# Kernel tuning notes

Hardware: AMD Instinct MI355X
Metric: run time of the kernel (lower is better)

The kernel has to match this reference:

```python
import jax, jax.numpy as jnp
import numpy as np
import itertools


def _rot24():
    # all 3x3 signed permutation matrices with det +1 -> 24 cube rotations
    mats = []
    I = np.eye(3)
    for perm in itertools.permutations(range(3)):
        P = I[list(perm)]
        for signs in itertools.product([1.0, -1.0], repeat=3):
            M = P * np.array(signs)[:, None]
            if np.linalg.det(M) > 0:
                mats.append(M)
    return np.stack(mats)  # (24, 3, 3)


def compute_spatial_pair_orbits():
    # O acts on the 24 positions (regular rep). Orbit of pair (i,j) under the
    # diagonal action g:(i,j)->(gi,gj) is indexed by the group element i^-1 j.
    R = _rot24()
    n = R.shape[0]
    orb = np.zeros((n, n), dtype=np.int64)
    for i in range(n):
        for j in range(n):
            M = R[i].T @ R[j]
            orb[i, j] = int(np.argmin(np.abs(R - M).sum(axis=(1, 2))))
    return orb, n  # (24, 24), 24 orbits


def compute_color_pair_orbits():
    # S6 on color pairs: orbit 0 = same color (a==b), orbit 1 = different
    a = np.arange(6)
    orb = (a[:, None] != a[None, :]).astype(np.int64)
    return orb, 2  # (6, 6), 2 orbits


K_IN = 64
K_OUT = 64
BATCH = 64


def setup_inputs() -> dict:
    key = jax.random.key(0)
    k_x, k_w = jax.random.split(key)
    sp_orbit_np, n_sp = compute_spatial_pair_orbits()
    co_orbit_np, n_co = compute_color_pair_orbits()
    x = jax.random.normal(k_x, (BATCH, 24, K_IN * 6), dtype=jnp.float32)
    # kaiming_uniform with a=sqrt(5): bound = sqrt(6 / ((1 + a^2) * fan_in)),
    # fan_in = k_in * n_sp * n_co (dims after the first of weight)
    fan_in = K_IN * n_sp * n_co
    bound = float(np.sqrt(6.0 / ((1.0 + 5.0) * fan_in)))
    weight = jax.random.uniform(k_w, (K_OUT, K_IN, n_sp, n_co),
                                dtype=jnp.float32, minval=-bound, maxval=bound)
    bias = jnp.zeros((K_OUT,), dtype=jnp.float32)
    return {
        "x": x,
        "weight": weight,
        "bias": bias,
        "sp_orbit": jnp.asarray(sp_orbit_np),
        "co_orbit": jnp.asarray(co_orbit_np),
    }


def reference(x, weight, bias, sp_orbit, co_orbit):
    B = x.shape[0]
    k_out, k_in = weight.shape[0], weight.shape[1]
    xr = x.reshape(B, 24, k_in, 6)                 # (B, j, ki, c)
    kernel = weight[:, :, sp_orbit, :]             # (ko, ki, 24, 24, n_co)
    kernel_full = kernel[:, :, :, :, co_orbit]     # (ko, ki, 24, 24, 6, 6)
    out = jnp.einsum('bjkc,okijdc->biod', xr, kernel_full)
    out = out + bias[None, None, :, None]
    return out.reshape(B, 24, k_out * 6)
```

## Files before the change

kernel.cpp:

```cpp
#include <hip/hip_runtime.h>


typedef short bf16x8 __attribute__((ext_vector_type(8)));
typedef float f32x4 __attribute__((ext_vector_type(4)));

static __device__ inline short f2bf(float f) {
    unsigned u = __builtin_bit_cast(unsigned, f);
    unsigned r = (u + 0x7fffu + ((u >> 16) & 1u)) >> 16;
    return (short)r;
}

#define MFMA16(a, b, c) __builtin_amdgcn_mfma_f32_16x16x32_bf16(a, b, c, 0, 0, 0)

__global__ __launch_bounds__(512) void prep_kernel(const float* __restrict__ weight,
                                                   const float* __restrict__ x,
                                                   short* __restrict__ Wfrag,
                                                   short* __restrict__ Bfrag) {
    __shared__ float xs[9216];
    __shared__ float Ss[1536];
    const int t = threadIdx.x;
    const int blk = blockIdx.x;

    if (blk < 24) {
        const int s = blk;
        const int o = t >> 3;
        const int k0 = (t & 7) << 3;
        bf16x8 vd, v1;
        #pragma unroll
        for (int e = 0; e < 8; ++e) {
            const float2 wv = *(const float2*)(weight + ((size_t)((o * 64 + k0 + e) * 24 + s) << 1));
            vd[e] = f2bf(wv.x - wv.y);
            v1[e] = f2bf(wv.y);
        }
        const int lane_f = (o & 15) | (((k0 >> 3) & 3) << 4);
        const int sub = ((o >> 4) * 2 + (k0 >> 5)) * 512 + lane_f * 8;
        *(bf16x8*)&Wfrag[(size_t)s * 4096 + sub] = vd;
        *(bf16x8*)&Wfrag[(size_t)(24 + s) * 4096 + sub] = v1;
    } else {
        const int b = blk - 24;
        const float4* xg = (const float4*)(x + (size_t)b * 9216);
        float4* x4 = (float4*)xs;
        for (int idx = t; idx < 2304; idx += 512) x4[idx] = xg[idx];
        __syncthreads();
        #pragma unroll
        for (int u = 0; u < 3; ++u) {
            const int idx = t + u * 512;
            const float* p = xs + idx * 6;
            Ss[idx] = ((p[0] + p[1]) + (p[2] + p[3])) + (p[4] + p[5]);
        }
        __syncthreads();
        for (int cid = t; cid < 2304; cid += 512) {
            const int d = cid / 384;
            const int kk = (cid - d * 384) * 8;
            bf16x8 v;
            if (kk < 1536) {
                #pragma unroll
                for (int e = 0; e < 8; ++e) v[e] = f2bf(xs[(kk + e) * 6 + d]);
            } else {
                const int jk = kk - 1536;
                #pragma unroll
                for (int e = 0; e < 8; ++e) v[e] = f2bf(Ss[jk + e]);
            }
            const int n = b * 6 + d;
            const int lane_f = (n & 15) | (((kk >> 3) & 3) << 4);
            *(bf16x8*)&Bfrag[(size_t)((n >> 4) * 96 + (kk >> 5)) * 512 + lane_f * 8] = v;
        }
    }
}

__global__ __launch_bounds__(512, 4) void gemm_kernel(const short* __restrict__ Wfrag,
                                                      const short* __restrict__ Bfrag,
                                                      const float* __restrict__ bias,
                                                      const int* __restrict__ sp,
                                                      float* __restrict__ out) {
    __shared__ __align__(16) float Red[8][64][16];

    const int tid = threadIdx.x;
    const int lane = tid & 63;
    const int w = tid >> 6;

    const int bx = (int)blockIdx.x;
    const int mt = bx % 48;
    const int nt = bx / 48;
    const int i  = mt >> 1;
    const int o0 = (mt & 1) * 32;
    const int n0 = nt * 32;

    const int p = w >> 2;
    const int jbase = (w & 3) * 6;

    int sidx[6];
    #pragma unroll
    for (int t_ = 0; t_ < 6; ++t_) sidx[t_] = sp[i * 24 + jbase + t_];

    const size_t abase0 = (size_t)p * 24 * 4096 + (size_t)(o0 >> 4) * 1024 + lane * 8;
    const short* bbase = Bfrag + (size_t)(n0 >> 4) * 49152 + (size_t)(p * 48 + jbase * 2) * 512 + lane * 8;

    f32x4 acc[2][2] = {{{0.f,0.f,0.f,0.f},{0.f,0.f,0.f,0.f}},
                       {{0.f,0.f,0.f,0.f},{0.f,0.f,0.f,0.f}}};

    bf16x8 rA[2][4], rB[2][4];

#define LOADSTEP(t_, buf)                                                       \
    {                                                                           \
        const short* ap = Wfrag + (size_t)sidx[t_] * 4096 + abase0;             \
        const short* bp = bbase + (t_) * 1024;                                  \
        _Pragma("unroll")                                                       \
        for (int f = 0; f < 4; ++f) {                                           \
            rA[buf][f] = *(const bf16x8*)(ap + f * 512);                        \
            rB[buf][f] = *(const bf16x8*)(bp + ((f >> 1) * 49152) + (f & 1) * 512); \
        }                                                                       \
    }

    LOADSTEP(0, 0)
    #pragma unroll
    for (int t_ = 0; t_ < 6; ++t_) {
        const int cur = t_ & 1;
        if (t_ < 5) LOADSTEP(t_ + 1, cur ^ 1)
        #pragma unroll
        for (int kc = 0; kc < 2; ++kc) {
            #pragma unroll
            for (int mi = 0; mi < 2; ++mi)
                #pragma unroll
                for (int ni = 0; ni < 2; ++ni)
                    acc[mi][ni] = MFMA16(rA[cur][mi * 2 + kc], rB[cur][ni * 2 + kc], acc[mi][ni]);
        }
    }
#undef LOADSTEP

    #pragma unroll
    for (int mi = 0; mi < 2; ++mi)
        #pragma unroll
        for (int ni = 0; ni < 2; ++ni)
            *(f32x4*)&Red[w][lane][mi * 8 + ni * 4] = acc[mi][ni];
    __syncthreads();

    if (tid < 256) {
        const int l  = tid & 63;
        const int g  = tid >> 6;
        const int mi = g >> 1;
        const int ni = g & 1;
        const int fb = mi * 8 + ni * 4;
        f32x4 sum = *(const f32x4*)&Red[0][l][fb];
        #pragma unroll
        for (int ww = 1; ww < 8; ++ww) sum += *(const f32x4*)&Red[ww][l][fb];

        const int col = n0 + ni * 16 + (l & 15);
        const int b = col / 6;
        const int d = col - b * 6;
        const int rb = (l >> 4) * 4;
        #pragma unroll
        for (int r = 0; r < 4; ++r) {
            const int o = o0 + mi * 16 + rb + r;
            out[((size_t)(b * 24 + i)) * 384 + o * 6 + d] = sum[r] + bias[o];
        }
    }
}

extern "C" void kernel_launch(void* const* d_in, const int* in_sizes, int n_in,
                              void* d_out, int out_size, void* d_ws, size_t ws_size,
                              hipStream_t stream) {
    const float* x      = (const float*)d_in[0];
    const float* weight = (const float*)d_in[1];
    const float* bias   = (const float*)d_in[2];
    const int*   sp     = (const int*)d_in[3];

    short* Wfrag = (short*)d_ws;
    short* Bfrag = Wfrag + (size_t)2 * 24 * 4096;

    prep_kernel<<<88, 512, 0, stream>>>(weight, x, Wfrag, Bfrag);
    gemm_kernel<<<576, 512, 0, stream>>>(Wfrag, Bfrag, bias, sp, (float*)d_out);
}
```

Measured before the change: 26.49 us.

## Split color-sum term into separate small GEMM shared across output colors

The color-sum term (weight for differing colors applied to the per-position color sum of x) does not depend on the output color. It is now computed once per batch in a separate small GEMM into a temporary T, instead of being repeated for every one of the six output colors inside the main GEMM. This halves the K dimension of the main GEMM, at the cost of an extra kernel launch and a global round-trip through T that the epilogue reads back.

```diff
diff --git a/kernel.cpp b/kernel.cpp
--- a/kernel.cpp
+++ b/kernel.cpp
@@ -15,7 +15,8 @@
 __global__ __launch_bounds__(512) void prep_kernel(const float* __restrict__ weight,
                                                    const float* __restrict__ x,
                                                    short* __restrict__ Wfrag,
-                                                   short* __restrict__ Bfrag) {
+                                                   short* __restrict__ BfragX,
+                                                   short* __restrict__ Sfrag) {
     __shared__ float xs[9216];
     __shared__ float Ss[1536];
     const int t = threadIdx.x;
@@ -49,30 +50,32 @@
             Ss[idx] = ((p[0] + p[1]) + (p[2] + p[3])) + (p[4] + p[5]);
         }
         __syncthreads();
-        for (int cid = t; cid < 2304; cid += 512) {
-            const int d = cid / 384;
-            const int kk = (cid - d * 384) * 8;
-            bf16x8 v;
-            if (kk < 1536) {
+        for (int cid = t; cid < 1344; cid += 512) {
+            if (cid < 1152) {
+                const int d = cid / 192;
+                const int kk = (cid - d * 192) * 8;
+                bf16x8 v;
                 #pragma unroll
                 for (int e = 0; e < 8; ++e) v[e] = f2bf(xs[(kk + e) * 6 + d]);
+                const int n = b * 6 + d;
+                const int lane_f = (n & 15) | (((kk >> 3) & 3) << 4);
+                *(bf16x8*)&BfragX[(size_t)((n >> 4) * 48 + (kk >> 5)) * 512 + lane_f * 8] = v;
             } else {
-                const int jk = kk - 1536;
-                #pragma unroll
-                for (int e = 0; e < 8; ++e) v[e] = f2bf(Ss[jk + e]);
+                const int kk = (cid - 1152) * 8;
+                bf16x8 v;
+                #pragma unroll
+                for (int e = 0; e < 8; ++e) v[e] = f2bf(Ss[kk + e]);
+                const int lane_f = (b & 15) | (((kk >> 3) & 3) << 4);
+                *(bf16x8*)&Sfrag[(size_t)((b >> 4) * 48 + (kk >> 5)) * 512 + lane_f * 8] = v;
             }
-            const int n = b * 6 + d;
-            const int lane_f = (n & 15) | (((kk >> 3) & 3) << 4);
-            *(bf16x8*)&Bfrag[(size_t)((n >> 4) * 96 + (kk >> 5)) * 512 + lane_f * 8] = v;
-        }
-    }
-}
-
-__global__ __launch_bounds__(512, 4) void gemm_kernel(const short* __restrict__ Wfrag,
-                                                      const short* __restrict__ Bfrag,
-                                                      const float* __restrict__ bias,
-                                                      const int* __restrict__ sp,
-                                                      float* __restrict__ out) {
+        }
+    }
+}
+
+__global__ __launch_bounds__(512, 4) void tgemm_kernel(const short* __restrict__ Wfrag,
+                                                       const short* __restrict__ Sfrag,
+                                                       const int* __restrict__ sp,
+                                                       float* __restrict__ T) {
     __shared__ __align__(16) float Red[8][64][16];
 
     const int tid = threadIdx.x;
@@ -81,24 +84,21 @@
 
     const int bx = (int)blockIdx.x;
     const int mt = bx % 48;
-    const int nt = bx / 48;
+    const int bt = bx / 48;
     const int i  = mt >> 1;
     const int o0 = (mt & 1) * 32;
-    const int n0 = nt * 32;
-
-    const int p = w >> 2;
-    const int jbase = (w & 3) * 6;
-
-    int sidx[6];
-    #pragma unroll
-    for (int t_ = 0; t_ < 6; ++t_) sidx[t_] = sp[i * 24 + jbase + t_];
-
-    const size_t abase0 = (size_t)p * 24 * 4096 + (size_t)(o0 >> 4) * 1024 + lane * 8;
-    const short* bbase = Bfrag + (size_t)(n0 >> 4) * 49152 + (size_t)(p * 48 + jbase * 2) * 512 + lane * 8;
+    const int n0 = bt * 32;
+
+    const int jbase = w * 3;
+    int sidx[3];
+    #pragma unroll
+    for (int t_ = 0; t_ < 3; ++t_) sidx[t_] = sp[i * 24 + jbase + t_];
+
+    const size_t abase0 = (size_t)24 * 4096 + (size_t)(o0 >> 4) * 1024 + lane * 8;
+    const short* bbase = Sfrag + (size_t)(n0 >> 4) * 24576 + (size_t)jbase * 1024 + lane * 8;
 
     f32x4 acc[2][2] = {{{0.f,0.f,0.f,0.f},{0.f,0.f,0.f,0.f}},
                        {{0.f,0.f,0.f,0.f},{0.f,0.f,0.f,0.f}}};
-
     bf16x8 rA[2][4], rB[2][4];
 
 #define LOADSTEP(t_, buf)                                                       \
@@ -108,23 +108,22 @@
         _Pragma("unroll")                                                       \
         for (int f = 0; f < 4; ++f) {                                           \
             rA[buf][f] = *(const bf16x8*)(ap + f * 512);                        \
-            rB[buf][f] = *(const bf16x8*)(bp + ((f >> 1) * 49152) + (f & 1) * 512); \
+            rB[buf][f] = *(const bf16x8*)(bp + ((f >> 1) * 24576) + (f & 1) * 512); \
         }                                                                       \
     }
 
     LOADSTEP(0, 0)
     #pragma unroll
-    for (int t_ = 0; t_ < 6; ++t_) {
+    for (int t_ = 0; t_ < 3; ++t_) {
         const int cur = t_ & 1;
-        if (t_ < 5) LOADSTEP(t_ + 1, cur ^ 1)
-        #pragma unroll
-        for (int kc = 0; kc < 2; ++kc) {
+        if (t_ < 2) LOADSTEP(t_ + 1, cur ^ 1)
+        #pragma unroll
+        for (int kc = 0; kc < 2; ++kc)
             #pragma unroll
             for (int mi = 0; mi < 2; ++mi)
                 #pragma unroll
                 for (int ni = 0; ni < 2; ++ni)
                     acc[mi][ni] = MFMA16(rA[cur][mi * 2 + kc], rB[cur][ni * 2 + kc], acc[mi][ni]);
-        }
     }
 #undef LOADSTEP
 
@@ -145,6 +144,90 @@
         #pragma unroll
         for (int ww = 1; ww < 8; ++ww) sum += *(const f32x4*)&Red[ww][l][fb];
 
+        const int b = n0 + ni * 16 + (l & 15);
+        const int rb = (l >> 4) * 4;
+        #pragma unroll
+        for (int r = 0; r < 4; ++r) {
+            const int o = o0 + mi * 16 + rb + r;
+            T[(size_t)(i * 64 + o) * 64 + b] = sum[r];
+        }
+    }
+}
+
+__global__ __launch_bounds__(512, 4) void gemm_kernel(const short* __restrict__ Wfrag,
+                                                      const short* __restrict__ BfragX,
+                                                      const float* __restrict__ T,
+                                                      const float* __restrict__ bias,
+                                                      const int* __restrict__ sp,
+                                                      float* __restrict__ out) {
+    __shared__ __align__(16) float Red[8][64][16];
+
+    const int tid = threadIdx.x;
+    const int lane = tid & 63;
+    const int w = tid >> 6;
+
+    const int bx = (int)blockIdx.x;
+    const int mt = bx % 48;
+    const int nt = bx / 48;
+    const int i  = mt >> 1;
+    const int o0 = (mt & 1) * 32;
+    const int n0 = nt * 32;
+
+    const int jbase = w * 3;
+    int sidx[3];
+    #pragma unroll
+    for (int t_ = 0; t_ < 3; ++t_) sidx[t_] = sp[i * 24 + jbase + t_];
+
+    const size_t abase0 = (size_t)(o0 >> 4) * 1024 + lane * 8;
+    const short* bbase = BfragX + (size_t)(n0 >> 4) * 24576 + (size_t)jbase * 1024 + lane * 8;
+
+    f32x4 acc[2][2] = {{{0.f,0.f,0.f,0.f},{0.f,0.f,0.f,0.f}},
+                       {{0.f,0.f,0.f,0.f},{0.f,0.f,0.f,0.f}}};
+    bf16x8 rA[2][4], rB[2][4];
+
+#define LOADSTEP(t_, buf)                                                       \
+    {                                                                           \
+        const short* ap = Wfrag + (size_t)sidx[t_] * 4096 + abase0;             \
+        const short* bp = bbase + (t_) * 1024;                                  \
+        _Pragma("unroll")                                                       \
+        for (int f = 0; f < 4; ++f) {                                           \
+            rA[buf][f] = *(const bf16x8*)(ap + f * 512);                        \
+            rB[buf][f] = *(const bf16x8*)(bp + ((f >> 1) * 24576) + (f & 1) * 512); \
+        }                                                                       \
+    }
+
+    LOADSTEP(0, 0)
+    #pragma unroll
+    for (int t_ = 0; t_ < 3; ++t_) {
+        const int cur = t_ & 1;
+        if (t_ < 2) LOADSTEP(t_ + 1, cur ^ 1)
+        #pragma unroll
+        for (int kc = 0; kc < 2; ++kc)
+            #pragma unroll
+            for (int mi = 0; mi < 2; ++mi)
+                #pragma unroll
+                for (int ni = 0; ni < 2; ++ni)
+                    acc[mi][ni] = MFMA16(rA[cur][mi * 2 + kc], rB[cur][ni * 2 + kc], acc[mi][ni]);
+    }
+#undef LOADSTEP
+
+    #pragma unroll
+    for (int mi = 0; mi < 2; ++mi)
+        #pragma unroll
+        for (int ni = 0; ni < 2; ++ni)
+            *(f32x4*)&Red[w][lane][mi * 8 + ni * 4] = acc[mi][ni];
+    __syncthreads();
+
+    if (tid < 256) {
+        const int l  = tid & 63;
+        const int g  = tid >> 6;
+        const int mi = g >> 1;
+        const int ni = g & 1;
+        const int fb = mi * 8 + ni * 4;
+        f32x4 sum = *(const f32x4*)&Red[0][l][fb];
+        #pragma unroll
+        for (int ww = 1; ww < 8; ++ww) sum += *(const f32x4*)&Red[ww][l][fb];
+
         const int col = n0 + ni * 16 + (l & 15);
         const int b = col / 6;
         const int d = col - b * 6;
@@ -152,7 +235,8 @@
         #pragma unroll
         for (int r = 0; r < 4; ++r) {
             const int o = o0 + mi * 16 + rb + r;
-            out[((size_t)(b * 24 + i)) * 384 + o * 6 + d] = sum[r] + bias[o];
+            const int m = i * 64 + o;
+            out[((size_t)(b * 24 + i)) * 384 + o * 6 + d] = sum[r] + T[(size_t)m * 64 + b] + bias[o];
         }
     }
 }
@@ -165,9 +249,12 @@
     const float* bias   = (const float*)d_in[2];
     const int*   sp     = (const int*)d_in[3];
 
-    short* Wfrag = (short*)d_ws;
-    short* Bfrag = Wfrag + (size_t)2 * 24 * 4096;
-
-    prep_kernel<<<88, 512, 0, stream>>>(weight, x, Wfrag, Bfrag);
-    gemm_kernel<<<576, 512, 0, stream>>>(Wfrag, Bfrag, bias, sp, (float*)d_out);
-}
+    short* Wfrag  = (short*)d_ws;
+    short* BfragX = Wfrag + 196608;
+    short* Sfrag  = BfragX + 589824;
+    float* T      = (float*)(Sfrag + 98304);
+
+    prep_kernel<<<88, 512, 0, stream>>>(weight, x, Wfrag, BfragX, Sfrag);
+    tgemm_kernel<<<96, 512, 0, stream>>>(Wfrag, Sfrag, sp, T);
+    gemm_kernel<<<576, 512, 0, stream>>>(Wfrag, BfragX, T, bias, sp, (float*)d_out);
+}
```

After: 24.34 us. 8.1% less time.

## Compute color-sum term once per batch instead of replicating across colors

Applied to the files above, without the earlier changes.

The before code packed the channel-summed input S into the B operand for every output color d, so the W1·S product was recomputed six times per batch column. It now stores S separately, one column per batch, and computes the W1·S term with a small extra MFMA accumulator. That result is broadcast to each color column in the reduction epilogue. The GEMM uses 256-thread blocks with 4 waves instead of 8 and a smaller LDS reduction, which lowers total MFMA work. In exchange each wave does more serial steps and there are extra scattered loads for the S fragments.

```diff
diff --git a/kernel.cpp b/kernel.cpp
--- a/kernel.cpp
+++ b/kernel.cpp
@@ -15,7 +15,8 @@
 __global__ __launch_bounds__(512) void prep_kernel(const float* __restrict__ weight,
                                                    const float* __restrict__ x,
                                                    short* __restrict__ Wfrag,
-                                                   short* __restrict__ Bfrag) {
+                                                   short* __restrict__ BfragX,
+                                                   short* __restrict__ Sfrag) {
     __shared__ float xs[9216];
     __shared__ float Ss[1536];
     const int t = threadIdx.x;
@@ -49,31 +50,36 @@
             Ss[idx] = ((p[0] + p[1]) + (p[2] + p[3])) + (p[4] + p[5]);
         }
         __syncthreads();
-        for (int cid = t; cid < 2304; cid += 512) {
-            const int d = cid / 384;
-            const int kk = (cid - d * 384) * 8;
-            bf16x8 v;
-            if (kk < 1536) {
+        for (int cid = t; cid < 1344; cid += 512) {
+            if (cid < 1152) {
+                const int d = cid / 192;
+                const int kk = (cid - d * 192) * 8;
+                bf16x8 v;
                 #pragma unroll
                 for (int e = 0; e < 8; ++e) v[e] = f2bf(xs[(kk + e) * 6 + d]);
+                const int n = b * 6 + d;
+                const int lane_f = (n & 15) | (((kk >> 3) & 3) << 4);
+                *(bf16x8*)&BfragX[(size_t)((n >> 4) * 48 + (kk >> 5)) * 512 + lane_f * 8] = v;
             } else {
-                const int jk = kk - 1536;
+                const int kk = (cid - 1152) * 8;
+                bf16x8 v;
                 #pragma unroll
-                for (int e = 0; e < 8; ++e) v[e] = f2bf(Ss[jk + e]);
+                for (int e = 0; e < 8; ++e) v[e] = f2bf(Ss[kk + e]);
+                const int lane_f = (b & 15) | (((kk >> 3) & 3) << 4);
+                *(bf16x8*)&Sfrag[(size_t)((b >> 4) * 48 + (kk >> 5)) * 512 + lane_f * 8] = v;
             }
-            const int n = b * 6 + d;
-            const int lane_f = (n & 15) | (((kk >> 3) & 3) << 4);
-            *(bf16x8*)&Bfrag[(size_t)((n >> 4) * 96 + (kk >> 5)) * 512 + lane_f * 8] = v;
-        }
-    }
-}
-
-__global__ __launch_bounds__(512, 4) void gemm_kernel(const short* __restrict__ Wfrag,
-                                                      const short* __restrict__ Bfrag,
+        }
+    }
+}
+
+__global__ __launch_bounds__(256, 3) void gemm_kernel(const short* __restrict__ Wfrag,
+                                                      const short* __restrict__ BfragX,
+                                                      const short* __restrict__ Sfrag,
                                                       const float* __restrict__ bias,
                                                       const int* __restrict__ sp,
                                                       float* __restrict__ out) {
-    __shared__ __align__(16) float Red[8][64][16];
+    __shared__ __align__(16) float RedM[4][64][16];
+    __shared__ __align__(16) float RedT[4][64][8];
 
     const int tid = threadIdx.x;
     const int lane = tid & 63;
@@ -85,20 +91,21 @@
     const int i  = mt >> 1;
     const int o0 = (mt & 1) * 32;
     const int n0 = nt * 32;
-
-    const int p = w >> 2;
-    const int jbase = (w & 3) * 6;
-
+    const int bg = nt / 3;
+
+    const int jbase = w * 6;
     int sidx[6];
     #pragma unroll
     for (int t_ = 0; t_ < 6; ++t_) sidx[t_] = sp[i * 24 + jbase + t_];
 
-    const size_t abase0 = (size_t)p * 24 * 4096 + (size_t)(o0 >> 4) * 1024 + lane * 8;
-    const short* bbase = Bfrag + (size_t)(n0 >> 4) * 49152 + (size_t)(p * 48 + jbase * 2) * 512 + lane * 8;
+    const size_t abase0  = (size_t)(o0 >> 4) * 1024 + lane * 8;
+    const size_t a1base0 = (size_t)24 * 4096 + abase0;
+    const short* bbase = BfragX + (size_t)(n0 >> 4) * 24576 + (size_t)jbase * 1024 + lane * 8;
+    const short* sbase = Sfrag  + (size_t)bg * 24576 + (size_t)jbase * 1024 + lane * 8;
 
     f32x4 acc[2][2] = {{{0.f,0.f,0.f,0.f},{0.f,0.f,0.f,0.f}},
                        {{0.f,0.f,0.f,0.f},{0.f,0.f,0.f,0.f}}};
-
+    f32x4 accT[2] = {{0.f,0.f,0.f,0.f},{0.f,0.f,0.f,0.f}};
     bf16x8 rA[2][4], rB[2][4];
 
 #define LOADSTEP(t_, buf)                                                       \
@@ -108,7 +115,7 @@
         _Pragma("unroll")                                                       \
         for (int f = 0; f < 4; ++f) {                                           \
             rA[buf][f] = *(const bf16x8*)(ap + f * 512);                        \
-            rB[buf][f] = *(const bf16x8*)(bp + ((f >> 1) * 49152) + (f & 1) * 512); \
+            rB[buf][f] = *(const bf16x8*)(bp + ((f >> 1) * 24576) + (f & 1) * 512); \
         }                                                                       \
     }
 
@@ -117,42 +124,67 @@
     for (int t_ = 0; t_ < 6; ++t_) {
         const int cur = t_ & 1;
         if (t_ < 5) LOADSTEP(t_ + 1, cur ^ 1)
-        #pragma unroll
-        for (int kc = 0; kc < 2; ++kc) {
+
+        bf16x8 rA1[4], rBs[2];
+        {
+            const short* a1p = Wfrag + (size_t)sidx[t_] * 4096 + a1base0;
+            const short* spp = sbase + t_ * 1024;
+            #pragma unroll
+            for (int f = 0; f < 4; ++f) rA1[f] = *(const bf16x8*)(a1p + f * 512);
+            rBs[0] = *(const bf16x8*)spp;
+            rBs[1] = *(const bf16x8*)(spp + 512);
+        }
+
+        #pragma unroll
+        for (int kc = 0; kc < 2; ++kc)
             #pragma unroll
             for (int mi = 0; mi < 2; ++mi)
                 #pragma unroll
                 for (int ni = 0; ni < 2; ++ni)
                     acc[mi][ni] = MFMA16(rA[cur][mi * 2 + kc], rB[cur][ni * 2 + kc], acc[mi][ni]);
-        }
+
+        #pragma unroll
+        for (int kc = 0; kc < 2; ++kc)
+            #pragma unroll
+            for (int mi = 0; mi < 2; ++mi)
+                accT[mi] = MFMA16(rA1[mi * 2 + kc], rBs[kc], accT[mi]);
     }
 #undef LOADSTEP
 
     #pragma unroll
-    for (int mi = 0; mi < 2; ++mi)
+    for (int mi = 0; mi < 2; ++mi) {
         #pragma unroll
         for (int ni = 0; ni < 2; ++ni)
-            *(f32x4*)&Red[w][lane][mi * 8 + ni * 4] = acc[mi][ni];
+            *(f32x4*)&RedM[w][lane][mi * 8 + ni * 4] = acc[mi][ni];
+        *(f32x4*)&RedT[w][lane][mi * 4] = accT[mi];
+    }
     __syncthreads();
 
-    if (tid < 256) {
+    {
         const int l  = tid & 63;
         const int g  = tid >> 6;
         const int mi = g >> 1;
         const int ni = g & 1;
         const int fb = mi * 8 + ni * 4;
-        f32x4 sum = *(const f32x4*)&Red[0][l][fb];
-        #pragma unroll
-        for (int ww = 1; ww < 8; ++ww) sum += *(const f32x4*)&Red[ww][l][fb];
+        f32x4 sum = *(const f32x4*)&RedM[0][l][fb];
+        #pragma unroll
+        for (int ww = 1; ww < 4; ++ww) sum += *(const f32x4*)&RedM[ww][l][fb];
 
         const int col = n0 + ni * 16 + (l & 15);
         const int b = col / 6;
         const int d = col - b * 6;
+        const int bcol = b - bg * 16;
+        const int lT = ((l >> 4) << 4) | bcol;
+        f32x4 ts = *(const f32x4*)&RedT[0][lT][mi * 4];
+        #pragma unroll
+        for (int ww = 1; ww < 4; ++ww) ts += *(const f32x4*)&RedT[ww][lT][mi * 4];
+
         const int rb = (l >> 4) * 4;
+        const int obase = o0 + mi * 16 + rb;
+        const f32x4 bv = *(const f32x4*)&bias[obase];
         #pragma unroll
         for (int r = 0; r < 4; ++r) {
-            const int o = o0 + mi * 16 + rb + r;
-            out[((size_t)(b * 24 + i)) * 384 + o * 6 + d] = sum[r] + bias[o];
+            out[((size_t)(b * 24 + i)) * 384 + (obase + r) * 6 + d] = sum[r] + ts[r] + bv[r];
         }
     }
 }
@@ -165,9 +197,10 @@
     const float* bias   = (const float*)d_in[2];
     const int*   sp     = (const int*)d_in[3];
 
-    short* Wfrag = (short*)d_ws;
-    short* Bfrag = Wfrag + (size_t)2 * 24 * 4096;
-
-    prep_kernel<<<88, 512, 0, stream>>>(weight, x, Wfrag, Bfrag);
-    gemm_kernel<<<576, 512, 0, stream>>>(Wfrag, Bfrag, bias, sp, (float*)d_out);
-}
+    short* Wfrag  = (short*)d_ws;
+    short* BfragX = Wfrag + 196608;
+    short* Sfrag  = BfragX + 589824;
+
+    prep_kernel<<<88, 512, 0, stream>>>(weight, x, Wfrag, BfragX, Sfrag);
+    gemm_kernel<<<576, 256, 0, stream>>>(Wfrag, BfragX, Sfrag, bias, sp, (float*)d_out);
+}
```

Measured after the change: 22.95 us. 1.15x faster.
